# Performance work log

Measured on AMD Instinct MI355X. Metric: run time of the kernel, lower is better.

Reference implementation:

```python
import jax, jax.numpy as jnp
import numpy as np

B, N, D, E, H = 2, 256, 512, 128, 4
NF, EF = 2048, 512
HD = D // H
SCALE = 1.0 / (3 * HD) ** 0.5

_LINS = [("qkv", D, 3 * D), ("rqk", E, 2 * H), ("nffn1", D, NF), ("nffn2", NF, D),
         ("o12", D, 2 * H), ("o3", H * H, E), ("t", E, 4 * H), ("t5", E, E),
         ("t6", H, E), ("effn1", E, EF), ("effn2", EF, E)]
_NORMS = [("n1", D), ("n2", D), ("en1", D), ("en2", E), ("en3", E)]


def _lin(k, din, dout):
    return (jax.random.normal(k, (din, dout), jnp.float32) / np.float32(np.sqrt(din)),
            jnp.zeros((dout,), jnp.float32))


def setup_inputs() -> dict:
    key = jax.random.key(0)
    ks = jax.random.split(key, 3 + len(_LINS))
    inp = {
        "x": jax.random.normal(ks[0], (B, N, D), jnp.float32),
        "p": jax.random.normal(ks[1], (B, N, N, E), jnp.float32),
        "attention_matrix_mask": jax.random.randint(ks[2], (B, N, N), 0, 2, jnp.int32),
    }
    for k, (name, din, dout) in zip(ks[3:], _LINS):
        inp[name + "_W"], inp[name + "_b"] = _lin(k, din, dout)
    for name, dim in _NORMS:
        inp[name + "_s"] = jnp.ones((dim,), jnp.float32)
        inp[name + "_b"] = jnp.zeros((dim,), jnp.float32)
    return inp


def _ln(x, s, b):
    m = jnp.mean(x, -1, keepdims=True)
    v = jnp.mean((x - m) ** 2, -1, keepdims=True)
    return (x - m) * jax.lax.rsqrt(v + 1e-5) * s + b


def reference(x, p, attention_matrix_mask,
              qkv_W, qkv_b, rqk_W, rqk_b, nffn1_W, nffn1_b, nffn2_W, nffn2_b,
              o12_W, o12_b, o3_W, o3_b, t_W, t_b, t5_W, t5_b, t6_W, t6_b,
              effn1_W, effn1_b, effn2_W, effn2_b,
              n1_s, n1_b, n2_s, n2_b, en1_s, en1_b, en2_s, en2_b, en3_s, en3_b):
    mask = attention_matrix_mask
    # ---- Node encoder layer (pre-LN) ----
    # NOTE: original code has `x + self.attention(...)` WITHOUT assignment, so the
    # attention output is discarded. We compute it for fidelity but do not use it.
    xn = _ln(x, n1_s, n1_b)
    qkv = (xn @ qkv_W + qkv_b).reshape(B, N, H, 3 * HD).transpose(0, 2, 1, 3)  # [B,H,N,3hd]
    q, k, v = jnp.split(qkv, 3, axis=-1)
    rqk = (p @ rqk_W + rqk_b).reshape(B, N, N, H, 2).transpose(0, 3, 1, 2, 4)  # [B,H,N,N,2]
    rq, rk = rqk[..., 0], rqk[..., 1]
    # (rq * k.unsqueeze(-2)).sum(-1) in torch reduces to rq[b,h,i,j] * sum_d k[b,h,i,d]
    scores = (jnp.einsum('bhid,bhjd->bhij', q, k)
              + rq * jnp.sum(k, -1)[..., None]
              + rk * jnp.sum(q, -1)[..., None])
    scores = jnp.where(mask[:, None] == 0, -10000.0, scores)
    probs = jax.nn.softmax(scores * SCALE, axis=-1)
    _attn_discarded = jnp.einsum('bhij,bhjd->bhid', probs, v).transpose(0, 2, 1, 3).reshape(B, N, D)
    # FFN residual (the only live update of x)
    x = x + jax.nn.gelu(_ln(x, n2_s, n2_b) @ nffn1_W + nffn1_b, approximate=False) @ nffn2_W + nffn2_b

    # ---- Edge encoder layer (pre-LN) ----
    # OuterProduct
    xn = _ln(x, en1_s, en1_b)
    o = xn @ o12_W + o12_b  # [B,N,2H]
    o1, o2 = o[..., :H], o[..., H:]
    op = jnp.einsum('bih,bjg->bijhg', o1, o2).reshape(B, N, N, H * H)
    p = p + op @ o3_W + o3_b
    # TriangularUpdate
    pn = _ln(p, en2_s, en2_b)
    tt = pn @ t_W + t_b  # [B,N,N,4H]; torch chunk(5) yields 4 chunks of size H when H<=4
    t1, t2, t3, t4 = jnp.split(tt, 4, axis=-1)
    t5 = pn @ t5_W + t5_b
    mb = (mask == 0)[..., None]
    t12 = jnp.where(mb, -10000.0, t1 * t2)
    t34 = jnp.where(mb, -10000.0, t3 * t4)
    a = jnp.sum(jax.nn.sigmoid(t12), axis=1)[:, None]   # [B,1,N,H]
    bsum = jnp.sum(jax.nn.sigmoid(t34), axis=2)[:, :, None]  # [B,N,1,H]
    og = a + bsum  # [B,N,N,H]
    t56 = jnp.where(mb, -10000.0, t5 * (og @ t6_W + t6_b))
    p = p + jax.nn.sigmoid(t56)
    # Edge FFN
    pn = _ln(p, en3_s, en3_b)
    p = p + jax.nn.gelu(pn @ effn1_W + effn1_b, approximate=False) @ effn2_W + effn2_b
    return (x, p)
```

## Files before the change

kernel.cpp:

```cpp
#include <hip/hip_runtime.h>
#include <hip/hip_bf16.h>

typedef __attribute__((ext_vector_type(8))) short s16x8;
typedef __attribute__((ext_vector_type(4))) float f32x4;
typedef __attribute__((ext_vector_type(4))) unsigned short us4;

#define DI __device__ __forceinline__

DI float b2f(unsigned short u){ union{float f; unsigned int i;} v; v.i = ((unsigned int)u)<<16; return v.f; }
DI unsigned short f2b(float f){ union{float f; unsigned int i;} v; v.f = f; unsigned int r = v.i + 0x7FFF + ((v.i>>16)&1u); return (unsigned short)(r>>16); }
DI float geluf(float x){ return 0.5f*x*(1.f + erff(x*0.70710678118654752f)); }
DI float sigmf(float x){ return 1.f/(1.f + expf(-x)); }

#define MFMA(a,b,c) __builtin_amdgcn_mfma_f32_16x16x32_bf16((a),(b),(c),0,0,0)

__global__ __launch_bounds__(256) void k_repack(const float* __restrict__ W,
                                                unsigned short* __restrict__ out,
                                                int M, int ktlog2, int total){
  int idx = blockIdx.x*256 + threadIdx.x;
  if(idx >= total) return;
  int j    = idx & 7;
  int lane = (idx>>3) & 63;
  int kt   = (idx>>9) & ((1<<ktlog2)-1);
  int mt   = idx >> (9+ktlog2);
  int k = kt*32 + (lane>>4)*8 + j;
  int m = mt*16 + (lane&15);
  out[idx] = f2b(W[k*M + m]);
}

__global__ __launch_bounds__(256) void k_repack2(const float* __restrict__ W,
                                                 unsigned short* __restrict__ oh,
                                                 unsigned short* __restrict__ ol,
                                                 int M, int ktlog2, int total){
  int idx = blockIdx.x*256 + threadIdx.x;
  if(idx >= total) return;
  int j    = idx & 7;
  int lane = (idx>>3) & 63;
  int kt   = (idx>>9) & ((1<<ktlog2)-1);
  int mt   = idx >> (9+ktlog2);
  int k = kt*32 + (lane>>4)*8 + j;
  int m = mt*16 + (lane&15);
  float v = W[k*M + m];
  unsigned short h = f2b(v);
  oh[idx] = h;
  ol[idx] = f2b(v - b2f(h));
}

__global__ __launch_bounds__(256) void k1_ln(const float* __restrict__ x,
                                             const float* __restrict__ s,
                                             const float* __restrict__ b,
                                             unsigned short* __restrict__ oh,
                                             unsigned short* __restrict__ ol){
  int row = blockIdx.x, t = threadIdx.x;
  const float* xr = x + row*512;
  float v0 = xr[t], v1 = xr[t+256];
  float sum = v0+v1, sq = v0*v0+v1*v1;
  for(int o=32;o>=1;o>>=1){ sum += __shfl_down(sum,o); sq += __shfl_down(sq,o); }
  __shared__ float ls[4], lq[4];
  int w = t>>6;
  if((t&63)==0){ ls[w]=sum; lq[w]=sq; }
  __syncthreads();
  sum = ls[0]+ls[1]+ls[2]+ls[3]; sq = lq[0]+lq[1]+lq[2]+lq[3];
  float m = sum*(1.f/512.f);
  float rstd = rsqrtf(sq*(1.f/512.f) - m*m + 1e-5f);
  float a0 = (v0-m)*rstd*s[t]     + b[t];
  float a1 = (v1-m)*rstd*s[t+256] + b[t+256];
  unsigned short h0 = f2b(a0), h1 = f2b(a1);
  oh[row*512+t]     = h0;  ol[row*512+t]     = f2b(a0 - b2f(h0));
  oh[row*512+t+256] = h1;  ol[row*512+t+256] = f2b(a1 - b2f(h1));
}

__global__ __launch_bounds__(256) void k2_ffn1(const unsigned short* __restrict__ xh,
                                               const unsigned short* __restrict__ xl,
                                               const unsigned short* __restrict__ Wh,
                                               const unsigned short* __restrict__ Wl,
                                               const float* __restrict__ b1,
                                               unsigned short* __restrict__ hh,
                                               unsigned short* __restrict__ hl){
  int t = threadIdx.x, w = t>>6, lane = t&63, l15 = lane&15, q = lane>>4;
  int rowbase = blockIdx.y*64;
  f32x4 acc[2][4];
  for(int a=0;a<2;a++) for(int n=0;n<4;n++) acc[a][n] = (f32x4){0.f,0.f,0.f,0.f};
  for(int kt=0;kt<16;kt++){
    s16x8 bh[4], bl[4];
    for(int nt=0;nt<4;nt++){
      int off = (rowbase + nt*16 + l15)*512 + kt*32 + q*8;
      bh[nt] = *(const s16x8*)(xh + off);
      bl[nt] = *(const s16x8*)(xl + off);
    }
    for(int mtl=0;mtl<2;mtl++){
      int mtg = blockIdx.x*8 + w*2 + mtl;
      int wi = ((mtg*16 + kt)*64 + lane)*8;
      s16x8 ah = *(const s16x8*)(Wh + wi);
      s16x8 al = *(const s16x8*)(Wl + wi);
      for(int nt=0;nt<4;nt++){
        acc[mtl][nt] = MFMA(ah, bh[nt], acc[mtl][nt]);
        acc[mtl][nt] = MFMA(ah, bl[nt], acc[mtl][nt]);
        acc[mtl][nt] = MFMA(al, bh[nt], acc[mtl][nt]);
      }
    }
  }
  for(int mtl=0;mtl<2;mtl++){
    int mtg = blockIdx.x*8 + w*2 + mtl;
    int col0 = mtg*16 + q*4;
    f32x4 bb = *(const f32x4*)(b1 + col0);
    for(int nt=0;nt<4;nt++){
      int row = rowbase + nt*16 + l15;
      us4 vh, vl;
      for(int r=0;r<4;r++){
        float g = geluf(acc[mtl][nt][r] + bb[r]);
        unsigned short h = f2b(g);
        vh[r] = h; vl[r] = f2b(g - b2f(h));
      }
      *(us4*)(hh + row*2048 + col0) = vh;
      *(us4*)(hl + row*2048 + col0) = vl;
    }
  }
}

__global__ __launch_bounds__(256) void k3_ffn2(const unsigned short* __restrict__ hh,
                                               const unsigned short* __restrict__ hl,
                                               const unsigned short* __restrict__ Wh,
                                               const unsigned short* __restrict__ Wl,
                                               const float* __restrict__ b2,
                                               const float* __restrict__ x,
                                               float* __restrict__ xout){
  int t = threadIdx.x, w = t>>6, lane = t&63, l15 = lane&15, q = lane>>4;
  int row = blockIdx.y*64 + w*16 + l15;
  f32x4 acc[2]; acc[0] = (f32x4){0.f,0.f,0.f,0.f}; acc[1] = acc[0];
  for(int kt=0;kt<64;kt++){
    int off = row*2048 + kt*32 + q*8;
    s16x8 bh = *(const s16x8*)(hh + off);
    s16x8 bl = *(const s16x8*)(hl + off);
    for(int mtl=0;mtl<2;mtl++){
      int mtg = blockIdx.x*2 + mtl;
      int wi = ((mtg*64 + kt)*64 + lane)*8;
      s16x8 ah = *(const s16x8*)(Wh + wi);
      s16x8 al = *(const s16x8*)(Wl + wi);
      acc[mtl] = MFMA(ah, bh, acc[mtl]);
      acc[mtl] = MFMA(ah, bl, acc[mtl]);
      acc[mtl] = MFMA(al, bh, acc[mtl]);
    }
  }
  for(int mtl=0;mtl<2;mtl++){
    int col0 = (blockIdx.x*2 + mtl)*16 + q*4;
    f32x4 xv = *(const f32x4*)(x + row*512 + col0);
    f32x4 bb = *(const f32x4*)(b2 + col0);
    f32x4 ov;
    for(int r=0;r<4;r++) ov[r] = xv[r] + acc[mtl][r] + bb[r];
    *(f32x4*)(xout + row*512 + col0) = ov;
  }
}

__global__ __launch_bounds__(256) void k4_o12(const float* __restrict__ xout,
                                              const float* __restrict__ s,
                                              const float* __restrict__ b,
                                              const float* __restrict__ o12W,
                                              const float* __restrict__ o12b,
                                              float* __restrict__ o1, float* __restrict__ o2){
  int row = blockIdx.x, t = threadIdx.x;
  const float* xr = xout + row*512;
  float v0 = xr[t], v1 = xr[t+256];
  float sum = v0+v1, sq = v0*v0+v1*v1;
  for(int o=32;o>=1;o>>=1){ sum += __shfl_down(sum,o); sq += __shfl_down(sq,o); }
  __shared__ float ls[4], lq[4];
  __shared__ float red[4][8];
  int w = t>>6;
  if((t&63)==0){ ls[w]=sum; lq[w]=sq; }
  __syncthreads();
  sum = ls[0]+ls[1]+ls[2]+ls[3]; sq = lq[0]+lq[1]+lq[2]+lq[3];
  float m = sum*(1.f/512.f);
  float rstd = rsqrtf(sq*(1.f/512.f) - m*m + 1e-5f);
  float x0 = (v0-m)*rstd*s[t]     + b[t];
  float x1 = (v1-m)*rstd*s[t+256] + b[t+256];
  f32x4 w0a = *(const f32x4*)(o12W + t*8),       w0b = *(const f32x4*)(o12W + t*8 + 4);
  f32x4 w1a = *(const f32x4*)(o12W + (t+256)*8), w1b = *(const f32x4*)(o12W + (t+256)*8 + 4);
  float pa[8];
  for(int r=0;r<4;r++){ pa[r]   = x0*w0a[r] + x1*w1a[r];
                        pa[4+r] = x0*w0b[r] + x1*w1b[r]; }
  for(int o=32;o>=1;o>>=1) for(int k=0;k<8;k++) pa[k] += __shfl_down(pa[k],o);
  if((t&63)==0) for(int k=0;k<8;k++) red[w][k] = pa[k];
  __syncthreads();
  if(t<8){
    float tot = red[0][t]+red[1][t]+red[2][t]+red[3][t] + o12b[t];
    if(t<4) o1[row*4+t] = tot; else o2[row*4+(t-4)] = tot;
  }
}

__global__ __launch_bounds__(256) void k5_p1(const float* __restrict__ p,
                                             const float* __restrict__ o3W,
                                             const float* __restrict__ o3b,
                                             const float* __restrict__ o1,
                                             const float* __restrict__ o2,
                                             float* __restrict__ p1){
  __shared__ float w_s[2048];
  __shared__ float b_s[128];
  int t = threadIdx.x;
  for(int r=0;r<8;r++) w_s[t*8+r] = o3W[t*8+r];
  if(t<128) b_s[t] = o3b[t];
  __syncthreads();
  int g = blockIdx.x*16 + (t>>4);
  int e0 = (t&15)*8;
  int bb = g>>16, ii = (g>>8)&255, jj = g&255;
  const float* o1p = o1 + (bb*256+ii)*4;
  const float* o2p = o2 + (bb*256+jj)*4;
  float c[16];
  for(int h=0;h<4;h++) for(int g2=0;g2<4;g2++) c[h*4+g2] = o1p[h]*o2p[g2];
  f32x4 pv0 = *(const f32x4*)(p + (long)g*128 + e0);
  f32x4 pv1 = *(const f32x4*)(p + (long)g*128 + e0 + 4);
  float acc[8];
  for(int r=0;r<4;r++){ acc[r] = pv0[r] + b_s[e0+r]; acc[4+r] = pv1[r] + b_s[e0+4+r]; }
  for(int m=0;m<16;m++){
    const float* wr = &w_s[m*128 + e0];
    for(int r=0;r<8;r++) acc[r] += c[m]*wr[r];
  }
  f32x4 s0, s1;
  for(int r=0;r<4;r++){ s0[r] = acc[r]; s1[r] = acc[4+r]; }
  *(f32x4*)(p1 + (long)g*128 + e0)     = s0;
  *(f32x4*)(p1 + (long)g*128 + e0 + 4) = s1;
}

DI void ln_stage64(const float* __restrict__ psrc,
                   const float* __restrict__ s2,
                   const float* __restrict__ b2,
                   unsigned short* pnh, unsigned short* pnl, int t){
  int lr = t>>2, qt = t&3, e0 = qt*32;
  const float* pr = psrc + lr*128 + e0;
  float v[32];
  for(int c=0;c<8;c++){ f32x4 u = *(const f32x4*)(pr + c*4); for(int r=0;r<4;r++) v[c*4+r] = u[r]; }
  float s = 0.f, sq = 0.f;
  for(int k=0;k<32;k++){ s += v[k]; sq += v[k]*v[k]; }
  s  += __shfl_xor(s,1);  s  += __shfl_xor(s,2);
  sq += __shfl_xor(sq,1); sq += __shfl_xor(sq,2);
  float m = s*(1.f/128.f);
  float rstd = rsqrtf(sq*(1.f/128.f) - m*m + 1e-5f);
  for(int c=0;c<8;c++){
    f32x4 sv = *(const f32x4*)(s2 + e0 + c*4), bv = *(const f32x4*)(b2 + e0 + c*4);
    us4 vh, vl;
    for(int r=0;r<4;r++){
      float val = (v[c*4+r]-m)*rstd*sv[r] + bv[r];
      unsigned short h = f2b(val);
      vh[r] = h; vl[r] = f2b(val - b2f(h));
    }
    *(us4*)&pnh[lr*136 + e0 + c*4] = vh;
    if(pnl) *(us4*)&pnl[lr*136 + e0 + c*4] = vl;
  }
}

__global__ __launch_bounds__(256) void k7a_tt(const float* __restrict__ p1,
                                              const float* __restrict__ en2s,
                                              const float* __restrict__ en2b,
                                              const unsigned short* __restrict__ tWT,
                                              const float* __restrict__ tb,
                                              const int* __restrict__ am,
                                              float* __restrict__ a_acc,
                                              float* __restrict__ bs_acc){
  __shared__ __align__(16) unsigned short pn[64*136];
  int t = threadIdx.x;
  long gbase = (long)blockIdx.x*64;
  ln_stage64(p1 + gbase*128, en2s, en2b, pn, (unsigned short*)0, t);
  __syncthreads();
  int w = t>>6, lane = t&63, l15 = lane&15, q = lane>>4;
  f32x4 acc = (f32x4){0.f,0.f,0.f,0.f};
  for(int kt=0;kt<4;kt++){
    s16x8 bf = *(const s16x8*)&pn[(w*16+l15)*136 + kt*32 + q*8];
    s16x8 af = *(const s16x8*)(tWT + (kt*64 + lane)*8);
    acc = MFMA(af, bf, acc);
  }
  f32x4 tb4 = *(const f32x4*)(tb + q*4);
  for(int r=0;r<4;r++) acc[r] += tb4[r];
  long g = gbase + w*16 + l15;
  int bb = (int)(g>>16), ii = ((int)g>>8)&255, jj = (int)g&255;
  int msk = am[(bb*256+ii)*256 + jj];
  float pr4[4];
  for(int r=0;r<4;r++) pr4[r] = __shfl_xor(acc[r], 16);
  if(msk){
    if(q==0){      for(int r=0;r<4;r++) atomicAdd(&a_acc[(bb*256+jj)*4+r],  sigmf(acc[r]*pr4[r])); }
    else if(q==2){ for(int r=0;r<4;r++) atomicAdd(&bs_acc[(bb*256+ii)*4+r], sigmf(acc[r]*pr4[r])); }
  }
}

__global__ __launch_bounds__(128) void k6b(const float* __restrict__ a_acc,
                                           const float* __restrict__ bs_acc,
                                           const float* __restrict__ t6W,
                                           const float* __restrict__ t6b,
                                           float* __restrict__ A2, float* __restrict__ Bs2){
  int d = blockIdx.x, e = threadIdx.x;
  float sa = 0.f, sb = 0.f;
  for(int h=0;h<4;h++){
    float wv = t6W[h*128+e];
    sa += a_acc[d*4+h]*wv;
    sb += bs_acc[d*4+h]*wv;
  }
  A2[d*128+e]  = sa;
  Bs2[d*128+e] = sb + t6b[e];
}

__global__ __launch_bounds__(256) void k7b_p2(float* __restrict__ dp,
                                              const float* __restrict__ en2s,
                                              const float* __restrict__ en2b,
                                              const unsigned short* __restrict__ t5Wh,
                                              const unsigned short* __restrict__ t5Wl,
                                              const float* __restrict__ t5b,
                                              const float* __restrict__ A2,
                                              const float* __restrict__ Bs2,
                                              const int* __restrict__ am){
  __shared__ __align__(16) unsigned short pnh[64*136];
  __shared__ __align__(16) unsigned short pnl[64*136];
  int t = threadIdx.x;
  long gbase = (long)blockIdx.x*64;
  ln_stage64(dp + gbase*128, en2s, en2b, pnh, pnl, t);
  __syncthreads();
  int w = t>>6, lane = t&63, l15 = lane&15, q = lane>>4;
  for(int mtl=0;mtl<2;mtl++){
    int mtg = w*2 + mtl;
    s16x8 afh[4], afl[4];
    for(int kt=0;kt<4;kt++){
      int wi = ((mtg*4+kt)*64 + lane)*8;
      afh[kt] = *(const s16x8*)(t5Wh + wi);
      afl[kt] = *(const s16x8*)(t5Wl + wi);
    }
    int e0 = mtg*16 + q*4;
    f32x4 t5b4 = *(const f32x4*)(t5b + e0);
    for(int nt=0;nt<4;nt++){
      f32x4 acc = (f32x4){0.f,0.f,0.f,0.f};
      for(int kt=0;kt<4;kt++){
        s16x8 bh = *(const s16x8*)&pnh[(nt*16+l15)*136 + kt*32 + q*8];
        s16x8 bl = *(const s16x8*)&pnl[(nt*16+l15)*136 + kt*32 + q*8];
        acc = MFMA(afh[kt], bh, acc);
        acc = MFMA(afh[kt], bl, acc);
        acc = MFMA(afl[kt], bh, acc);
      }
      long g = gbase + nt*16 + l15;
      int bb = (int)(g>>16), ii = ((int)g>>8)&255, jj = (int)g&255;
      int msk = am[(bb*256+ii)*256 + jj];
      const float* A2p = A2 + (bb*256+jj)*128 + e0;
      const float* Bsp = Bs2 + (bb*256+ii)*128 + e0;
      f32x4 p1v = *(const f32x4*)(dp + g*128 + e0);
      f32x4 ov;
      for(int r=0;r<4;r++){
        float sg = 0.f;
        if(msk){
          float t56 = (acc[r] + t5b4[r]) * (A2p[r] + Bsp[r]);
          sg = sigmf(t56);
        }
        ov[r] = p1v[r] + sg;
      }
      *(f32x4*)(dp + g*128 + e0) = ov;
    }
  }
}

__global__ __launch_bounds__(256) void k8_effn(float* __restrict__ dp,
                                               const float* __restrict__ en3s,
                                               const float* __restrict__ en3b,
                                               const unsigned short* __restrict__ W1T,
                                               const float* __restrict__ b1,
                                               const unsigned short* __restrict__ W2T,
                                               const float* __restrict__ b2){
  __shared__ __align__(16) unsigned short pn3[32*136];
  __shared__ __align__(16) unsigned short hT[32*520];
  int t = threadIdx.x;
  long base = (long)blockIdx.x*32;
  {
    int lr = t>>3, oct = t&7, e0 = oct*16;
    const float* pr = dp + (base+lr)*128 + e0;
    float v[16];
    for(int c=0;c<4;c++){ f32x4 u = *(const f32x4*)(pr + c*4); for(int r=0;r<4;r++) v[c*4+r] = u[r]; }
    float s = 0.f, sq = 0.f;
    for(int k=0;k<16;k++){ s += v[k]; sq += v[k]*v[k]; }
    s  += __shfl_xor(s,1);  s  += __shfl_xor(s,2);  s  += __shfl_xor(s,4);
    sq += __shfl_xor(sq,1); sq += __shfl_xor(sq,2); sq += __shfl_xor(sq,4);
    float m = s*(1.f/128.f);
    float rstd = rsqrtf(sq*(1.f/128.f) - m*m + 1e-5f);
    for(int c=0;c<4;c++){
      f32x4 sv = *(const f32x4*)(en3s + e0 + c*4), bv = *(const f32x4*)(en3b + e0 + c*4);
      us4 ov;
      for(int r=0;r<4;r++) ov[r] = f2b((v[c*4+r]-m)*rstd*sv[r] + bv[r]);
      *(us4*)&pn3[lr*136 + e0 + c*4] = ov;
    }
  }
  __syncthreads();
  int w = t>>6, lane = t&63, l15 = lane&15, q = lane>>4;
  {
    s16x8 bfr[2][4];
    for(int nt=0;nt<2;nt++) for(int kt=0;kt<4;kt++)
      bfr[nt][kt] = *(const s16x8*)&pn3[(nt*16+l15)*136 + kt*32 + q*8];
    for(int mtl=0;mtl<8;mtl++){
      int mtg = w*8 + mtl;
      s16x8 af[4];
      for(int kt=0;kt<4;kt++) af[kt] = *(const s16x8*)(W1T + ((mtg*4+kt)*64 + lane)*8);
      int col0 = mtg*16 + q*4;
      f32x4 bb = *(const f32x4*)(b1 + col0);
      for(int nt=0;nt<2;nt++){
        f32x4 acc = (f32x4){0.f,0.f,0.f,0.f};
        for(int kt=0;kt<4;kt++) acc = MFMA(af[kt], bfr[nt][kt], acc);
        us4 hv;
        for(int r=0;r<4;r++) hv[r] = f2b(geluf(acc[r] + bb[r]));
        *(us4*)&hT[(nt*16+l15)*520 + col0] = hv;
      }
    }
  }
  __syncthreads();
  {
    f32x4 acc2[2][2];
    for(int a=0;a<2;a++) for(int n=0;n<2;n++) acc2[a][n] = (f32x4){0.f,0.f,0.f,0.f};
    for(int kt=0;kt<16;kt++){
      s16x8 bfr[2];
      for(int nt=0;nt<2;nt++) bfr[nt] = *(const s16x8*)&hT[(nt*16+l15)*520 + kt*32 + q*8];
      for(int mtl=0;mtl<2;mtl++){
        int m2 = w*2 + mtl;
        s16x8 af = *(const s16x8*)(W2T + ((m2*16+kt)*64 + lane)*8);
        for(int nt=0;nt<2;nt++) acc2[mtl][nt] = MFMA(af, bfr[nt], acc2[mtl][nt]);
      }
    }
    for(int mtl=0;mtl<2;mtl++){
      int m2 = w*2 + mtl;
      int col0 = m2*16 + q*4;
      f32x4 bb = *(const f32x4*)(b2 + col0);
      for(int nt=0;nt<2;nt++){
        long g = base + nt*16 + l15;
        f32x4 p2v = *(const f32x4*)(dp + g*128 + col0);
        f32x4 ov;
        for(int r=0;r<4;r++) ov[r] = p2v[r] + acc2[mtl][nt][r] + bb[r];
        *(f32x4*)(dp + g*128 + col0) = ov;
      }
    }
  }
}

extern "C" void kernel_launch(void* const* d_in, const int* in_sizes, int n_in,
                              void* d_out, int out_size, void* d_ws, size_t ws_size,
                              hipStream_t stream) {
  const float* x      = (const float*)d_in[0];
  const float* p      = (const float*)d_in[1];
  const int*   am     = (const int*)d_in[2];
  const float* nffn1W = (const float*)d_in[7];
  const float* nffn1b = (const float*)d_in[8];
  const float* nffn2W = (const float*)d_in[9];
  const float* nffn2b = (const float*)d_in[10];
  const float* o12W   = (const float*)d_in[11];
  const float* o12b   = (const float*)d_in[12];
  const float* o3W    = (const float*)d_in[13];
  const float* o3b    = (const float*)d_in[14];
  const float* tW     = (const float*)d_in[15];
  const float* tb     = (const float*)d_in[16];
  const float* t5W    = (const float*)d_in[17];
  const float* t5b    = (const float*)d_in[18];
  const float* t6W    = (const float*)d_in[19];
  const float* t6b    = (const float*)d_in[20];
  const float* e1W    = (const float*)d_in[21];
  const float* e1b    = (const float*)d_in[22];
  const float* e2W    = (const float*)d_in[23];
  const float* e2b    = (const float*)d_in[24];
  const float* n2s    = (const float*)d_in[27];
  const float* n2b    = (const float*)d_in[28];
  const float* en1s   = (const float*)d_in[29];
  const float* en1b   = (const float*)d_in[30];
  const float* en2s   = (const float*)d_in[31];
  const float* en2b   = (const float*)d_in[32];
  const float* en3s   = (const float*)d_in[33];
  const float* en3b   = (const float*)d_in[34];

  float* ox  = (float*)d_out;
  float* opx = (float*)d_out + 262144;

  char* ws = (char*)d_ws;
  float* a_acc  = (float*)(ws + 0);
  float* bs_acc = (float*)(ws + 8192);
  float* o1w    = (float*)(ws + 16384);
  float* o2w    = (float*)(ws + 24576);
  float* A2     = (float*)(ws + 32768);
  float* Bs2    = (float*)(ws + 294912);
  unsigned short* xnh = (unsigned short*)(ws + 557056);
  unsigned short* xnl = (unsigned short*)(ws + 1081344);
  unsigned short* h1h = (unsigned short*)(ws + 1605632);
  unsigned short* h1l = (unsigned short*)(ws + 3702784);
  unsigned short* tWT  = (unsigned short*)(ws + 5799936);
  unsigned short* t5Wh = (unsigned short*)(ws + 5804032);
  unsigned short* t5Wl = (unsigned short*)(ws + 5836800);
  unsigned short* W1T  = (unsigned short*)(ws + 5869568);
  unsigned short* W2T  = (unsigned short*)(ws + 6000640);
  unsigned short* n1h  = (unsigned short*)(ws + 6131712);
  unsigned short* n1l  = (unsigned short*)(ws + 8228864);
  unsigned short* n2h  = (unsigned short*)(ws + 10326016);
  unsigned short* n2l  = (unsigned short*)(ws + 12423168);

  hipMemsetAsync(ws, 0, 16384, stream);

  k_repack <<<2048/256,    256, 0, stream>>>(tW,  tWT,  16,  2, 2048);
  k_repack2<<<16384/256,   256, 0, stream>>>(t5W, t5Wh, t5Wl, 128, 2, 16384);
  k_repack <<<65536/256,   256, 0, stream>>>(e1W, W1T,  512, 2, 65536);
  k_repack <<<65536/256,   256, 0, stream>>>(e2W, W2T,  128, 4, 65536);
  k_repack2<<<1048576/256, 256, 0, stream>>>(nffn1W, n1h, n1l, 2048, 4, 1048576);
  k_repack2<<<1048576/256, 256, 0, stream>>>(nffn2W, n2h, n2l, 512,  6, 1048576);

  k1_ln<<<512, 256, 0, stream>>>(x, n2s, n2b, xnh, xnl);
  k2_ffn1<<<dim3(16,8), 256, 0, stream>>>(xnh, xnl, n1h, n1l, nffn1b, h1h, h1l);
  k3_ffn2<<<dim3(16,8), 256, 0, stream>>>(h1h, h1l, n2h, n2l, nffn2b, x, ox);
  k4_o12<<<512, 256, 0, stream>>>(ox, en1s, en1b, o12W, o12b, o1w, o2w);

  k5_p1<<<8192, 256, 0, stream>>>(p, o3W, o3b, o1w, o2w, opx);
  k7a_tt<<<2048, 256, 0, stream>>>(opx, en2s, en2b, tWT, tb, am, a_acc, bs_acc);
  k6b<<<512, 128, 0, stream>>>(a_acc, bs_acc, t6W, t6b, A2, Bs2);
  k7b_p2<<<2048, 256, 0, stream>>>(opx, en2s, en2b, t5Wh, t5Wl, t5b, A2, Bs2, am);
  k8_effn<<<4096, 256, 0, stream>>>(opx, en3s, en3b, W1T, e1b, W2T, e2b);
}
```

Baseline: 584.9 us.

## Replace atomic triangular sums with 8x8 tiled partials and vectorize weight repack

The triangular-update kernel now processes 8x8 (i,j) tiles per block and reduces the masked sigmoid sums in shared memory. Each block writes per-tile partials, which k6b then sums over the 32 groups. This removes the global atomicAdds and the workspace memset. Separately, the weight repack kernels now have each thread convert 8 consecutive k values and store them as one 16-byte vector, which cuts the thread count by 8x. The cost is an extra partial-sum pass and a less contiguous row mapping in the LN stage.

```diff
diff --git a/kernel.cpp b/kernel.cpp
--- a/kernel.cpp
+++ b/kernel.cpp
@@ -16,34 +16,39 @@
 
 __global__ __launch_bounds__(256) void k_repack(const float* __restrict__ W,
                                                 unsigned short* __restrict__ out,
-                                                int M, int ktlog2, int total){
+                                                int M, int ktlog2, int nthreads){
   int idx = blockIdx.x*256 + threadIdx.x;
-  if(idx >= total) return;
-  int j    = idx & 7;
-  int lane = (idx>>3) & 63;
-  int kt   = (idx>>9) & ((1<<ktlog2)-1);
-  int mt   = idx >> (9+ktlog2);
-  int k = kt*32 + (lane>>4)*8 + j;
-  int m = mt*16 + (lane&15);
-  out[idx] = f2b(W[k*M + m]);
+  if(idx >= nthreads) return;
+  int lane = idx & 63;
+  int kt   = (idx>>6) & ((1<<ktlog2)-1);
+  int mt   = idx >> (6+ktlog2);
+  int k0 = kt*32 + (lane>>4)*8;
+  int m  = mt*16 + (lane&15);
+  s16x8 o;
+  for(int j=0;j<8;j++) o[j] = (short)f2b(W[(k0+j)*M + m]);
+  *(s16x8*)(out + (long)idx*8) = o;
 }
 
 __global__ __launch_bounds__(256) void k_repack2(const float* __restrict__ W,
                                                  unsigned short* __restrict__ oh,
                                                  unsigned short* __restrict__ ol,
-                                                 int M, int ktlog2, int total){
+                                                 int M, int ktlog2, int nthreads){
   int idx = blockIdx.x*256 + threadIdx.x;
-  if(idx >= total) return;
-  int j    = idx & 7;
-  int lane = (idx>>3) & 63;
-  int kt   = (idx>>9) & ((1<<ktlog2)-1);
-  int mt   = idx >> (9+ktlog2);
-  int k = kt*32 + (lane>>4)*8 + j;
-  int m = mt*16 + (lane&15);
-  float v = W[k*M + m];
-  unsigned short h = f2b(v);
-  oh[idx] = h;
-  ol[idx] = f2b(v - b2f(h));
+  if(idx >= nthreads) return;
+  int lane = idx & 63;
+  int kt   = (idx>>6) & ((1<<ktlog2)-1);
+  int mt   = idx >> (6+ktlog2);
+  int k0 = kt*32 + (lane>>4)*8;
+  int m  = mt*16 + (lane&15);
+  s16x8 vh, vl;
+  for(int j=0;j<8;j++){
+    float v = W[(k0+j)*M + m];
+    unsigned short h = f2b(v);
+    vh[j] = (short)h;
+    vl[j] = (short)f2b(v - b2f(h));
+  }
+  *(s16x8*)(oh + (long)idx*8) = vh;
+  *(s16x8*)(ol + (long)idx*8) = vl;
 }
 
 __global__ __launch_bounds__(256) void k1_ln(const float* __restrict__ x,
@@ -253,12 +258,33 @@
                                               const unsigned short* __restrict__ tWT,
                                               const float* __restrict__ tb,
                                               const int* __restrict__ am,
-                                              float* __restrict__ a_acc,
-                                              float* __restrict__ bs_acc){
+                                              float* __restrict__ a_part,
+                                              float* __restrict__ bs_part){
   __shared__ __align__(16) unsigned short pn[64*136];
+  __shared__ float sga[64][4];
+  __shared__ float sgb[64][4];
   int t = threadIdx.x;
-  long gbase = (long)blockIdx.x*64;
-  ln_stage64(p1 + gbase*128, en2s, en2b, pn, (unsigned short*)0, t);
+  int jjt = blockIdx.x & 31, iig = (blockIdx.x>>5) & 31, bb = blockIdx.x>>10;
+  {
+    int lr = t>>2, qt = t&3, e0 = qt*32;
+    int di = lr>>3, dj = lr&7;
+    long g = (long)bb*65536 + (iig*8+di)*256 + (jjt*8+dj);
+    const float* pr = p1 + g*128 + e0;
+    float v[32];
+    for(int c=0;c<8;c++){ f32x4 u = *(const f32x4*)(pr + c*4); for(int r=0;r<4;r++) v[c*4+r] = u[r]; }
+    float s = 0.f, sq = 0.f;
+    for(int k=0;k<32;k++){ s += v[k]; sq += v[k]*v[k]; }
+    s  += __shfl_xor(s,1);  s  += __shfl_xor(s,2);
+    sq += __shfl_xor(sq,1); sq += __shfl_xor(sq,2);
+    float m = s*(1.f/128.f);
+    float rstd = rsqrtf(sq*(1.f/128.f) - m*m + 1e-5f);
+    for(int c=0;c<8;c++){
+      f32x4 sv = *(const f32x4*)(en2s + e0 + c*4), bv = *(const f32x4*)(en2b + e0 + c*4);
+      us4 ov;
+      for(int r=0;r<4;r++) ov[r] = f2b((v[c*4+r]-m)*rstd*sv[r] + bv[r]);
+      *(us4*)&pn[lr*136 + e0 + c*4] = ov;
+    }
+  }
   __syncthreads();
   int w = t>>6, lane = t&63, l15 = lane&15, q = lane>>4;
   f32x4 acc = (f32x4){0.f,0.f,0.f,0.f};
@@ -269,28 +295,52 @@
   }
   f32x4 tb4 = *(const f32x4*)(tb + q*4);
   for(int r=0;r<4;r++) acc[r] += tb4[r];
-  long g = gbase + w*16 + l15;
-  int bb = (int)(g>>16), ii = ((int)g>>8)&255, jj = (int)g&255;
-  int msk = am[(bb*256+ii)*256 + jj];
+  int rloc = w*16 + l15;
+  int di = rloc>>3, dj = rloc&7;
+  int msk = am[(bb*256 + iig*8+di)*256 + jjt*8+dj];
   float pr4[4];
   for(int r=0;r<4;r++) pr4[r] = __shfl_xor(acc[r], 16);
-  if(msk){
-    if(q==0){      for(int r=0;r<4;r++) atomicAdd(&a_acc[(bb*256+jj)*4+r],  sigmf(acc[r]*pr4[r])); }
-    else if(q==2){ for(int r=0;r<4;r++) atomicAdd(&bs_acc[(bb*256+ii)*4+r], sigmf(acc[r]*pr4[r])); }
-  }
-}
-
-__global__ __launch_bounds__(128) void k6b(const float* __restrict__ a_acc,
-                                           const float* __restrict__ bs_acc,
+  if(q==0){      for(int r=0;r<4;r++) sga[rloc][r] = msk ? sigmf(acc[r]*pr4[r]) : 0.f; }
+  else if(q==2){ for(int r=0;r<4;r++) sgb[rloc][r] = msk ? sigmf(acc[r]*pr4[r]) : 0.f; }
+  __syncthreads();
+  if(t < 32){
+    int djr = t>>2, r = t&3;
+    float s = 0.f;
+    for(int d=0;d<8;d++) s += sga[d*8+djr][r];
+    a_part[(((long)bb*32+iig)*256 + jjt*8+djr)*4 + r] = s;
+  } else if(t < 64){
+    int dir = (t-32)>>2, r = t&3;
+    float s = 0.f;
+    for(int d=0;d<8;d++) s += sgb[dir*8+d][r];
+    bs_part[(((long)bb*32+jjt)*256 + iig*8+dir)*4 + r] = s;
+  }
+}
+
+__global__ __launch_bounds__(128) void k6b(const float* __restrict__ a_part,
+                                           const float* __restrict__ bs_part,
                                            const float* __restrict__ t6W,
                                            const float* __restrict__ t6b,
                                            float* __restrict__ A2, float* __restrict__ Bs2){
-  int d = blockIdx.x, e = threadIdx.x;
+  int d = blockIdx.x;
+  int bb = d>>8, rw = d&255;
+  int e = threadIdx.x;
+  __shared__ float as[4], bsr[4];
+  if(e < 4){
+    float s = 0.f;
+    for(int g=0;g<32;g++) s += a_part[(((long)bb*32+g)*256 + rw)*4 + e];
+    as[e] = s;
+  } else if(e < 8){
+    int r = e-4;
+    float s = 0.f;
+    for(int g=0;g<32;g++) s += bs_part[(((long)bb*32+g)*256 + rw)*4 + r];
+    bsr[r] = s;
+  }
+  __syncthreads();
   float sa = 0.f, sb = 0.f;
   for(int h=0;h<4;h++){
     float wv = t6W[h*128+e];
-    sa += a_acc[d*4+h]*wv;
-    sb += bs_acc[d*4+h]*wv;
+    sa += as[h]*wv;
+    sb += bsr[h]*wv;
   }
   A2[d*128+e]  = sa;
   Bs2[d*128+e] = sb + t6b[e];
@@ -466,8 +516,6 @@
   float* opx = (float*)d_out + 262144;
 
   char* ws = (char*)d_ws;
-  float* a_acc  = (float*)(ws + 0);
-  float* bs_acc = (float*)(ws + 8192);
   float* o1w    = (float*)(ws + 16384);
   float* o2w    = (float*)(ws + 24576);
   float* A2     = (float*)(ws + 32768);
@@ -485,15 +533,15 @@
   unsigned short* n1l  = (unsigned short*)(ws + 8228864);
   unsigned short* n2h  = (unsigned short*)(ws + 10326016);
   unsigned short* n2l  = (unsigned short*)(ws + 12423168);
-
-  hipMemsetAsync(ws, 0, 16384, stream);
-
-  k_repack <<<2048/256,    256, 0, stream>>>(tW,  tWT,  16,  2, 2048);
-  k_repack2<<<16384/256,   256, 0, stream>>>(t5W, t5Wh, t5Wl, 128, 2, 16384);
-  k_repack <<<65536/256,   256, 0, stream>>>(e1W, W1T,  512, 2, 65536);
-  k_repack <<<65536/256,   256, 0, stream>>>(e2W, W2T,  128, 4, 65536);
-  k_repack2<<<1048576/256, 256, 0, stream>>>(nffn1W, n1h, n1l, 2048, 4, 1048576);
-  k_repack2<<<1048576/256, 256, 0, stream>>>(nffn2W, n2h, n2l, 512,  6, 1048576);
+  float* a_part  = (float*)(ws + 14520320);
+  float* bs_part = (float*)(ws + 14782464);
+
+  k_repack <<<1,   256, 0, stream>>>(tW,  tWT,  16,  2, 256);
+  k_repack2<<<8,   256, 0, stream>>>(t5W, t5Wh, t5Wl, 128, 2, 2048);
+  k_repack <<<32,  256, 0, stream>>>(e1W, W1T,  512, 2, 8192);
+  k_repack <<<32,  256, 0, stream>>>(e2W, W2T,  128, 4, 8192);
+  k_repack2<<<512, 256, 0, stream>>>(nffn1W, n1h, n1l, 2048, 4, 131072);
+  k_repack2<<<512, 256, 0, stream>>>(nffn2W, n2h, n2l, 512,  6, 131072);
 
   k1_ln<<<512, 256, 0, stream>>>(x, n2s, n2b, xnh, xnl);
   k2_ffn1<<<dim3(16,8), 256, 0, stream>>>(xnh, xnl, n1h, n1l, nffn1b, h1h, h1l);
@@ -501,8 +549,8 @@
   k4_o12<<<512, 256, 0, stream>>>(ox, en1s, en1b, o12W, o12b, o1w, o2w);
 
   k5_p1<<<8192, 256, 0, stream>>>(p, o3W, o3b, o1w, o2w, opx);
-  k7a_tt<<<2048, 256, 0, stream>>>(opx, en2s, en2b, tWT, tb, am, a_acc, bs_acc);
-  k6b<<<512, 128, 0, stream>>>(a_acc, bs_acc, t6W, t6b, A2, Bs2);
+  k7a_tt<<<2048, 256, 0, stream>>>(opx, en2s, en2b, tWT, tb, am, a_part, bs_part);
+  k6b<<<512, 128, 0, stream>>>(a_part, bs_part, t6W, t6b, A2, Bs2);
   k7b_p2<<<2048, 256, 0, stream>>>(opx, en2s, en2b, t5Wh, t5Wl, t5b, A2, Bs2, am);
   k8_effn<<<4096, 256, 0, stream>>>(opx, en3s, en3b, W1T, e1b, W2T, e2b);
 }
```

After: 495.5 us. 15.3% less time.
